# Performance work log

Measured on AMD Instinct MI355X. Metric: run time of the kernel, lower is better.

Reference implementation:

```python
import jax, jax.numpy as jnp
import numpy as np

B, T, C = 2, 2048, 2048
NH, HS = 16, 128          # heads, head_size = C // NH
NLQ, NLKV = 512, 512      # q / kv latent dims
DHR = 64                  # decoupled rope head dim


def _rope_cos_sin(T, dhr, dtype=jnp.float32):
    inv = 1.0 / (10000.0 ** (np.arange(0, dhr, 2, dtype=np.float32) / dhr))
    ang = np.arange(T, dtype=np.float32)[:, None] * inv[None, :]  # [T, dhr//2]
    return jnp.asarray(np.cos(ang), dtype), jnp.asarray(np.sin(ang), dtype)


def setup_inputs() -> dict:
    key = jax.random.key(0)
    ks = jax.random.split(key, 10)
    s = 0.02
    cos, sin = _rope_cos_sin(T, DHR)
    return {
        "x":     jax.random.normal(ks[0], (B, T, C), jnp.float32),
        "cos":   cos,
        "sin":   sin,
        "W_dq":  s * jax.random.normal(ks[1], (NLQ, C), jnp.float32),
        "W_uq":  s * jax.random.normal(ks[2], (C, NLQ), jnp.float32),
        "W_dkv": s * jax.random.normal(ks[3], (NLKV, C), jnp.float32),
        "W_uk":  s * jax.random.normal(ks[4], (C, NLKV), jnp.float32),
        "W_uv":  s * jax.random.normal(ks[5], (C, NLKV), jnp.float32),
        "W_qr":  s * jax.random.normal(ks[6], (NH * DHR, NLQ), jnp.float32),
        "W_kr":  s * jax.random.normal(ks[7], (DHR, C), jnp.float32),
        "W_o":   s * jax.random.normal(ks[8], (C, C), jnp.float32),
    }


def _apply_rope(x, cos, sin):
    # x: [B, T, H, D]; pairs are interleaved (even=real, odd=imag)
    xr = x.reshape(x.shape[:-1] + (-1, 2))
    re, im = xr[..., 0], xr[..., 1]
    c = cos[None, :, None, :]
    s = sin[None, :, None, :]
    out = jnp.stack([re * c - im * s, re * s + im * c], axis=-1)
    return out.reshape(x.shape)


def reference(x, cos, sin, W_dq, W_uq, W_dkv, W_uk, W_uv, W_qr, W_kr, W_o):
    b, t, c = x.shape
    nh, hs, nlq, nlkv, dhr = NH, HS, NLQ, NLKV, DHR
    scale = 1.0 / np.sqrt(hs + dhr).astype(np.float32)

    # low-rank latents
    c_q = x @ W_dq.T          # [B, T, nlq]
    c_kv = x @ W_dkv.T        # [B, T, nlkv]

    # absorbed matrices (training path)
    # W_uq: [C, nlq] viewed as [nlq, nh, hs]; W_uk: [C, nlkv] viewed as [nh, hs, nlkv]
    k_eff = jnp.einsum('qhd,hdk->hqk', W_uq.reshape(nlq, nh, hs),
                       W_uk.reshape(nh, hs, nlkv))              # [nh, nlq, nlkv]
    v_eff = (W_uv.T @ W_o.T).reshape(nlkv, nh, hs).transpose(1, 0, 2)  # [nh, nlkv, hs]

    # content scores via absorbed low-rank path
    qk = jnp.einsum('btq,hqk->bhtk', c_q, k_eff)                # [B, nh, T, nlkv]
    attn_c = jnp.einsum('bhtk,bsk->bhts', qk, c_kv)             # [B, nh, T, T]

    # decoupled RoPE scores
    c_kr = (x @ W_kr.T)[:, :, None, :]                          # [B, T, 1, dhr]
    k_r = _apply_rope(c_kr, cos, sin)[:, :, 0, :]               # [B, T, dhr]
    c_qr = (c_q @ W_qr.T).reshape(b, t, nh, dhr)
    q_r = _apply_rope(c_qr, cos, sin)                            # [B, T, nh, dhr]
    attn_r = jnp.einsum('bthd,bsd->bhts', q_r, k_r)             # [B, nh, T, T]

    attn = (attn_c + attn_r) * scale
    mask = jnp.tril(jnp.ones((t, t), dtype=bool))
    attn = jnp.where(mask[None, None], attn, -jnp.inf)
    p = jax.nn.softmax(attn, axis=-1)

    ctx = jnp.einsum('bhts,bsk->bhtk', p, c_kv)                 # [B, nh, T, nlkv]
    y = jnp.einsum('bhtk,hkd->bthd', ctx, v_eff).reshape(b, t, c)
    return y
```

## Files before the change

### kernel.cpp

```cpp
#include <hip/hip_runtime.h>
#include <hip/hip_bf16.h>
#include <math.h>

typedef long long ll;
typedef unsigned short ushort_t;
typedef __attribute__((ext_vector_type(8))) __bf16 bf16x8;
typedef __attribute__((ext_vector_type(4))) float f32x4;

__device__ __forceinline__ ushort_t f2bf(float f) {
    __hip_bfloat16 h = __float2bfloat16(f);
    return *reinterpret_cast<ushort_t*>(&h);
}
__device__ __forceinline__ float bf2f(ushort_t u) {
    return __uint_as_float(((unsigned)u) << 16);
}
__device__ __forceinline__ void stage16(const void* g_lane, void* lds_uniform) {
    __builtin_amdgcn_global_load_lds(
        (const __attribute__((address_space(1))) unsigned int*)g_lane,
        (__attribute__((address_space(3))) unsigned int*)lds_uniform, 16, 0, 0);
}

#define DPPMAX(v, ctrl) v = fmaxf(v, __uint_as_float((unsigned)__builtin_amdgcn_update_dpp( \
        0, (int)__float_as_uint(v), (ctrl), 0xF, 0xF, true)))
#define DPPADD(v, ctrl) v = v + __uint_as_float((unsigned)__builtin_amdgcn_update_dpp( \
        0, (int)__float_as_uint(v), (ctrl), 0xF, 0xF, true))
__device__ __forceinline__ float red_max16(float v) {
    DPPMAX(v, 0xB1); DPPMAX(v, 0x4E); DPPMAX(v, 0x141); DPPMAX(v, 0x140); return v;
}
__device__ __forceinline__ float red_sum16(float v) {
    DPPADD(v, 0xB1); DPPADD(v, 0x4E); DPPADD(v, 0x141); DPPADD(v, 0x140); return v;
}

#define TM 128
#define TN 128
#define TK 64

__global__ __launch_bounds__(256)
void gemm_bf16(const ushort_t* __restrict__ Ab, const ushort_t* __restrict__ Bb,
               void* __restrict__ Cb,
               int M, int N, int K,
               int a_rs, int b_rs, int c_rs, int Z2,
               ll a_bs1, ll a_bs2, ll b_bs1, ll b_bs2, ll c_bs1, ll c_bs2,
               int out_f32)
{
    const int m0 = blockIdx.y * TM;
    const int n0 = blockIdx.x * TN;
    const int z1 = blockIdx.z / Z2, z2 = blockIdx.z % Z2;

    const ushort_t* A = Ab + z1 * a_bs1 + z2 * a_bs2;
    const ushort_t* B = Bb + z1 * b_bs1 + z2 * b_bs2;

    __shared__ ushort_t As[2][TM][TK];
    __shared__ ushort_t Bs[2][TN][TK];

    const int tid  = threadIdx.x;
    const int w    = tid >> 6;
    const int l    = tid & 63;
    const int lo16 = l & 15;
    const int quad = l >> 4;
    const int wm0  = (w & 1) * 64;
    const int wn0  = (w >> 1) * 64;

    const int srow  = l >> 3;
    const int sunit = (l & 7) ^ srow;

    f32x4 acc[4][4];
    const f32x4 zero = {0.f, 0.f, 0.f, 0.f};
#pragma unroll
    for (int mi = 0; mi < 4; ++mi)
#pragma unroll
        for (int nj = 0; nj < 4; ++nj) acc[mi][nj] = zero;

    const int nIter = K / TK;

#pragma unroll
    for (int i = 0; i < 4; ++i) {
        const int rr = w * 32 + i * 8;
        stage16(A + (ll)(m0 + rr + srow) * a_rs + sunit * 8, &As[0][rr][0]);
        stage16(B + (ll)(n0 + rr + srow) * b_rs + sunit * 8, &Bs[0][rr][0]);
    }

    int buf = 0;
    for (int it = 0; it < nIter; ++it) {
        __syncthreads();
        if (it + 1 < nIter) {
            const int k0 = (it + 1) * TK;
            const int nb = buf ^ 1;
#pragma unroll
            for (int i = 0; i < 4; ++i) {
                const int rr = w * 32 + i * 8;
                stage16(A + (ll)(m0 + rr + srow) * a_rs + (k0 + sunit * 8), &As[nb][rr][0]);
                stage16(B + (ll)(n0 + rr + srow) * b_rs + (k0 + sunit * 8), &Bs[nb][rr][0]);
            }
        }
#pragma unroll
        for (int h = 0; h < 2; ++h) {
            const int phys = (h * 4 + quad) ^ (lo16 & 7);
            bf16x8 af[4], bfr[4];
#pragma unroll
            for (int mi = 0; mi < 4; ++mi)
                af[mi] = *(const bf16x8*)&As[buf][wm0 + mi * 16 + lo16][phys * 8];
#pragma unroll
            for (int nj = 0; nj < 4; ++nj)
                bfr[nj] = *(const bf16x8*)&Bs[buf][wn0 + nj * 16 + lo16][phys * 8];
#pragma unroll
            for (int mi = 0; mi < 4; ++mi)
#pragma unroll
                for (int nj = 0; nj < 4; ++nj)
                    acc[mi][nj] = __builtin_amdgcn_mfma_f32_16x16x32_bf16(
                        af[mi], bfr[nj], acc[mi][nj], 0, 0, 0);
        }
        buf ^= 1;
    }

    if (out_f32) {
        float* C = (float*)Cb + z1 * c_bs1 + z2 * c_bs2;
#pragma unroll
        for (int mi = 0; mi < 4; ++mi)
#pragma unroll
            for (int r = 0; r < 4; ++r) {
                const ll row = m0 + wm0 + mi * 16 + quad * 4 + r;
                float* cr = C + row * (ll)c_rs + (n0 + wn0 + lo16);
#pragma unroll
                for (int nj = 0; nj < 4; ++nj) cr[nj * 16] = acc[mi][nj][r];
            }
    } else {
        ushort_t* C = (ushort_t*)Cb + z1 * c_bs1 + z2 * c_bs2;
#pragma unroll
        for (int mi = 0; mi < 4; ++mi)
#pragma unroll
            for (int r = 0; r < 4; ++r) {
                const ll row = m0 + wm0 + mi * 16 + quad * 4 + r;
                ushort_t* cr = C + row * (ll)c_rs + (n0 + wn0 + lo16);
#pragma unroll
                for (int nj = 0; nj < 4; ++nj) cr[nj * 16] = f2bf(acc[mi][nj][r]);
            }
    }
}

#define QP_RS 3072
#define XP_RS 1152

__global__ __launch_bounds__(512)
void flash_mla(const ushort_t* __restrict__ QP,
               const ushort_t* __restrict__ WukT,
               const ushort_t* __restrict__ XP,
               const ushort_t* __restrict__ VT,
               float* __restrict__ out,
               float scale)
{
    const int h  = blockIdx.y;
    const int b  = blockIdx.z;

    __shared__ __align__(16) char smem[98304];
    ushort_t* Bw = (ushort_t*)smem;
    ushort_t* Q3 = (ushort_t*)(smem + 16384);

    const int tid  = threadIdx.x;
    const int w    = tid >> 6;
    const int g    = w >> 2;
    const int wl   = w & 3;
    const int l    = tid & 63;
    const int lo16 = l & 15;
    const int quad = l >> 4;
    char* Pw = smem + 90112 + w * 1024;

#pragma unroll 1
    for (int task = 0; task < 2; ++task) {
        const int jj = task ? (int)blockIdx.x : 15 - (int)blockIdx.x;
        const int qt = 2 * jj + g;
        const int t0 = qt * 64;
        const int nst = 4 * jj + 4;
        const int myLast = 2 * qt + (wl >> 1);

        __syncthreads();

        bf16x8 qa[18];

#pragma unroll
        for (int i = 0; i < 2; ++i) {
            int p = w * 128 + i * 64 + l;
            int r = p >> 4, u = p & 15, ul = u ^ (r & 15);
            stage16(WukT + ((ll)h * 512 + r) * 128 + ul * 8,
                    (char*)Bw + (ll)(w * 128 + i * 64) * 16);
        }
        bf16x8 ab[4];
#pragma unroll
        for (int kd = 0; kd < 4; ++kd)
            ab[kd] = *(const bf16x8*)(QP + (ll)(b * 2048 + t0 + 16 * wl + lo16) * QP_RS +
                                      h * 128 + kd * 32 + quad * 8);
        __syncthreads();

        for (int kc = 0; kc < 8; ++kc) {
#pragma unroll
            for (int nt = 0; nt < 4; ++nt) {
                f32x4 c = {0.f, 0.f, 0.f, 0.f};
#pragma unroll
                for (int kd = 0; kd < 4; ++kd) {
                    bf16x8 bb = *(const bf16x8*)(Bw + (nt * 16 + lo16) * 128 +
                                                 (((kd * 4 + quad) ^ lo16) & 15) * 8);
                    c = __builtin_amdgcn_mfma_f32_16x16x32_bf16(ab[kd], bb, c, 0, 0, 0);
                }
#pragma unroll
                for (int r = 0; r < 4; ++r)
                    Q3[(w * 16 + quad * 4 + r) * 72 + nt * 16 + lo16] = f2bf(c[r]);
            }
#pragma unroll
            for (int kd2 = 0; kd2 < 2; ++kd2)
                qa[kc * 2 + kd2] = *(const bf16x8*)(Q3 + (w * 16 + lo16) * 72 + kd2 * 32 + quad * 8);

            if (kc < 7) {
                __syncthreads();
#pragma unroll
                for (int i = 0; i < 2; ++i) {
                    int p = w * 128 + i * 64 + l;
                    int r = p >> 4, u = p & 15, ul = u ^ (r & 15);
                    stage16(WukT + ((ll)h * 512 + (kc + 1) * 64 + r) * 128 + ul * 8,
                            (char*)Bw + (ll)(w * 128 + i * 64) * 16);
                }
                __syncthreads();
            }
        }
#pragma unroll
        for (int kt = 16; kt < 18; ++kt)
            qa[kt] = *(const bf16x8*)(QP + (ll)(b * 2048 + t0 + 16 * wl + lo16) * QP_RS +
                                      2048 + h * 64 + (kt - 16) * 32 + quad * 8);

        f32x4 oacc[8];
        const f32x4 zero = {0.f, 0.f, 0.f, 0.f};
#pragma unroll
        for (int dt = 0; dt < 8; ++dt) oacc[dt] = zero;
        float mrow[4], lrow[4];
#pragma unroll
        for (int r = 0; r < 4; ++r) { mrow[r] = -3.0e38f; lrow[r] = 0.f; }

        __syncthreads();

        if (w < 6) {
#pragma unroll
            for (int i = 0; i < 6; ++i) {
                int p = w * 384 + i * 64 + l;
                int r = p / 72, u = p % 72, ul = u ^ (r & 7);
                stage16(XP + (ll)(b * 2048 + r) * XP_RS + 512 + ul * 8,
                        smem + (ll)(w * 384 + i * 64) * 16);
            }
        } else {
#pragma unroll
            for (int i = 0; i < 4; ++i) {
                int p = (w - 6) * 256 + i * 64 + l;
                int r = p >> 2, u = p & 3, ul = u ^ (r & 3);
                stage16(VT + ((ll)(b * 16 + h) * 128 + r) * 2048 + ul * 8,
                        smem + 73728 + (ll)((w - 6) * 256 + i * 64) * 16);
            }
        }

        int buf = 0;
        for (int st = 0; st < nst; ++st) {
            __syncthreads();

            if (st + 1 < nst) {
                const int s0n = (st + 1) * 32;
                const int nb = buf ^ 1;
                if (w < 6) {
                    char* ksn = smem + nb * 36864;
#pragma unroll
                    for (int i = 0; i < 6; ++i) {
                        int p = w * 384 + i * 64 + l;
                        int r = p / 72, u = p % 72, ul = u ^ (r & 7);
                        stage16(XP + (ll)(b * 2048 + s0n + r) * XP_RS + 512 + ul * 8,
                                ksn + (ll)(w * 384 + i * 64) * 16);
                    }
                } else {
                    char* vsn = smem + 73728 + nb * 8192;
#pragma unroll
                    for (int i = 0; i < 4; ++i) {
                        int p = (w - 6) * 256 + i * 64 + l;
                        int r = p >> 2, u = p & 3, ul = u ^ (r & 3);
                        stage16(VT + ((ll)(b * 16 + h) * 128 + r) * 2048 + s0n + ul * 8,
                                vsn + (ll)((w - 6) * 256 + i * 64) * 16);
                    }
                }
            }

            if (st <= myLast) {
                const int s0 = st * 32;
                const ushort_t* Ks = (const ushort_t*)(smem + buf * 36864);
                const ushort_t* Vs = (const ushort_t*)(smem + 73728 + buf * 8192);

                f32x4 sc[2];
                sc[0] = zero; sc[1] = zero;
                __builtin_amdgcn_s_setprio(1);
#pragma unroll
                for (int kt = 0; kt < 18; ++kt)
#pragma unroll
                    for (int nt = 0; nt < 2; ++nt) {
                        int phys = (kt * 4 + quad) ^ (lo16 & 7);
                        bf16x8 kb = *(const bf16x8*)(Ks + (nt * 16 + lo16) * 576 + phys * 8);
                        sc[nt] = __builtin_amdgcn_mfma_f32_16x16x32_bf16(qa[kt], kb, sc[nt], 0, 0, 0);
                    }
                __builtin_amdgcn_s_setprio(0);

                const int rbase = 16 * wl + quad * 4;
#pragma unroll
                for (int nt = 0; nt < 2; ++nt)
#pragma unroll
                    for (int r = 0; r < 4; ++r) sc[nt][r] *= scale;
                if (st >= 2 * qt) {
#pragma unroll
                    for (int nt = 0; nt < 2; ++nt)
#pragma unroll
                        for (int r = 0; r < 4; ++r)
                            if ((s0 + nt * 16 + lo16) > (t0 + rbase + r))
                                sc[nt][r] = -INFINITY;
                }

                float alpha[4];
#pragma unroll
                for (int r = 0; r < 4; ++r) {
                    float tm = red_max16(fmaxf(sc[0][r], sc[1][r]));
                    float mnew = fmaxf(mrow[r], tm);
                    alpha[r] = __expf(mrow[r] - mnew);
                    mrow[r] = mnew;
                    sc[0][r] = __expf(sc[0][r] - mnew);
                    sc[1][r] = __expf(sc[1][r] - mnew);
                    float rs = red_sum16(sc[0][r] + sc[1][r]);
                    lrow[r] = lrow[r] * alpha[r] + rs;
                }
#pragma unroll
                for (int dt = 0; dt < 8; ++dt)
#pragma unroll
                    for (int r = 0; r < 4; ++r) oacc[dt][r] *= alpha[r];

#pragma unroll
                for (int nt = 0; nt < 2; ++nt)
#pragma unroll
                    for (int r = 0; r < 4; ++r) {
                        int row = quad * 4 + r;
                        int col = nt * 16 + lo16;
                        *(ushort_t*)(Pw + row * 64 + (((col >> 3) ^ (row & 3)) << 4) + (col & 7) * 2)
                            = f2bf(sc[nt][r]);
                    }
                bf16x8 pf = *(const bf16x8*)(Pw + lo16 * 64 + (quad ^ (lo16 & 3)) * 16);

                __builtin_amdgcn_s_setprio(1);
#pragma unroll
                for (int dt = 0; dt < 8; ++dt) {
                    int phys = quad ^ (lo16 & 3);
                    bf16x8 vb = *(const bf16x8*)(Vs + (dt * 16 + lo16) * 32 + phys * 8);
                    oacc[dt] = __builtin_amdgcn_mfma_f32_16x16x32_bf16(pf, vb, oacc[dt], 0, 0, 0);
                }
                __builtin_amdgcn_s_setprio(0);
            }
            buf ^= 1;
        }

#pragma unroll
        for (int r = 0; r < 4; ++r) {
            const float inv = 1.0f / lrow[r];
            const ll row = (ll)(b * 2048 + t0 + 16 * wl + quad * 4 + r);
#pragma unroll
            for (int dt = 0; dt < 8; ++dt)
                out[row * 2048 + h * 128 + dt * 16 + lo16] = oacc[dt][r] * inv;
        }
    }
}

__global__ void cvt_f32_bf16(const float* __restrict__ in, ushort_t* __restrict__ out, ll n4)
{
    ll i = (ll)blockIdx.x * 256 + threadIdx.x;
    if (i >= n4) return;
    float4 v = *(const float4*)(in + i * 4);
    ushort4 u;
    u.x = f2bf(v.x); u.y = f2bf(v.y); u.z = f2bf(v.z); u.w = f2bf(v.w);
    *(ushort4*)(out + i * 4) = u;
}

__global__ void build_wb1(const float* __restrict__ Wdq, const float* __restrict__ Wdkv,
                          const float* __restrict__ Wkr, ushort_t* __restrict__ out)
{
    ll i4 = ((ll)blockIdx.x * 256 + threadIdx.x) * 4;
    if (i4 >= (ll)1152 * 2048) return;
    int row = (int)(i4 >> 11);
    int col = (int)(i4 & 2047);
    float4 v = make_float4(0.f, 0.f, 0.f, 0.f);
    if (row < 512)       v = *(const float4*)(Wdq + (ll)row * 2048 + col);
    else if (row < 1024) v = *(const float4*)(Wdkv + (ll)(row - 512) * 2048 + col);
    else if (row < 1088) v = *(const float4*)(Wkr + (ll)(row - 1024) * 2048 + col);
    ushort4 u;
    u.x = f2bf(v.x); u.y = f2bf(v.y); u.z = f2bf(v.z); u.w = f2bf(v.w);
    *(ushort4*)(out + i4) = u;
}

__global__ void transpose_f32_bf16(const float* __restrict__ in, ushort_t* __restrict__ out,
                                   int R, int C, ll in_bs, ll out_bs)
{
    __shared__ float tile[32][33];
    const float* I = in + (ll)blockIdx.z * in_bs;
    ushort_t*    O = out + (ll)blockIdx.z * out_bs;
    int r0 = blockIdx.y * 32, c0 = blockIdx.x * 32;
    int tx = threadIdx.x & 31, ty = threadIdx.x >> 5;
#pragma unroll
    for (int i = 0; i < 4; ++i)
        tile[ty + i * 8][tx] = I[(ll)(r0 + ty + i * 8) * C + (c0 + tx)];
    __syncthreads();
#pragma unroll
    for (int i = 0; i < 4; ++i)
        O[(ll)(c0 + ty + i * 8) * R + (r0 + tx)] = f2bf(tile[tx][ty + i * 8]);
}

__global__ void rope_kr(ushort_t* __restrict__ XP, const float* __restrict__ cb,
                        const float* __restrict__ sb)
{
    int idx = blockIdx.x * 256 + threadIdx.x;
    if (idx >= 2 * 2048 * 32) return;
    int j = idx & 31, t = (idx >> 5) & 2047, b = idx >> 16;
    float c = cb[t * 32 + j], s = sb[t * 32 + j];
    ushort_t* p = XP + ((ll)(b * 2048 + t)) * 1152 + 1024 + 2 * j;
    float re = bf2f(p[0]), im = bf2f(p[1]);
    p[0] = f2bf(re * c - im * s);
    p[1] = f2bf(re * s + im * c);
}

__global__ void rope_qr_ip(ushort_t* __restrict__ QP, const float* __restrict__ cb,
                           const float* __restrict__ sb)
{
    int idx = blockIdx.x * 256 + threadIdx.x;
    if (idx >= 4096 * 512) return;
    int pj = idx & 511, h = pj >> 5, j = pj & 31;
    int row = idx >> 9;
    int t = row & 2047;
    float c = cb[t * 32 + j], s = sb[t * 32 + j];
    ll base = (ll)row * 3072 + 2048 + h * 64 + 2 * j;
    float re = bf2f(QP[base]), im = bf2f(QP[base + 1]);
    QP[base]     = f2bf(re * c - im * s);
    QP[base + 1] = f2bf(re * s + im * c);
}

static inline void gemmb(hipStream_t st, const ushort_t* A, const ushort_t* B, void* C,
                         int M, int N, int K, int a_rs, int b_rs, int c_rs,
                         int nb, int Z2,
                         ll a_bs1, ll a_bs2, ll b_bs1, ll b_bs2, ll c_bs1, ll c_bs2,
                         int of32)
{
    dim3 g(N / TN, M / TM, nb);
    gemm_bf16<<<g, 256, 0, st>>>(A, B, C, M, N, K, a_rs, b_rs, c_rs, Z2,
                                 a_bs1, a_bs2, b_bs1, b_bs2, c_bs1, c_bs2, of32);
}

extern "C" void kernel_launch(void* const* d_in, const int* in_sizes, int n_in,
                              void* d_out, int out_size, void* d_ws, size_t ws_size,
                              hipStream_t stream)
{
    const float* x     = (const float*)d_in[0];
    const float* cosb  = (const float*)d_in[1];
    const float* sinb  = (const float*)d_in[2];
    const float* W_dq  = (const float*)d_in[3];
    const float* W_uq  = (const float*)d_in[4];
    const float* W_dkv = (const float*)d_in[5];
    const float* W_uk  = (const float*)d_in[6];
    const float* W_uv  = (const float*)d_in[7];
    const float* W_qr  = (const float*)d_in[8];
    const float* W_kr  = (const float*)d_in[9];
    const float* W_o   = (const float*)d_in[10];
    float* out = (float*)d_out;

    const float scale = 0.07216878364870323f;

    char* base = (char*)d_ws;
    ushort_t* WB1     = (ushort_t*)(base + 0);
    ushort_t* WukT_b  = (ushort_t*)(base + 4718592);
    ushort_t* WuvT_b  = (ushort_t*)(base + 6815744);
    ushort_t* WB2     = (ushort_t*)(base + 8912896);
    ushort_t* veffT_b = (ushort_t*)(base + 12058624);
    ushort_t* Wo_b    = (ushort_t*)(base + 14155776);
    ushort_t* xb      = (ushort_t*)(base + 22544384);
    ushort_t* XP      = (ushort_t*)(base + 39321600);
    ushort_t* VT_all  = (ushort_t*)(base + 48758784);
    ushort_t* QP      = (ushort_t*)(base + 65536000);

    cvt_f32_bf16<<<8192, 256, 0, stream>>>(x, xb, 2097152);
    cvt_f32_bf16<<<4096, 256, 0, stream>>>(W_o, Wo_b, 1048576);
    build_wb1<<<2304, 256, 0, stream>>>(W_dq, W_dkv, W_kr, WB1);
    transpose_f32_bf16<<<dim3(16, 4, 16), 256, 0, stream>>>(W_uk, WukT_b, 128, 512, 65536, 65536);
    transpose_f32_bf16<<<dim3(16, 64, 1), 256, 0, stream>>>(W_uv, WuvT_b, 2048, 512, 0, 0);
    transpose_f32_bf16<<<dim3(64, 16, 1), 256, 0, stream>>>(W_uq, WB2, 512, 2048, 0, 0);
    cvt_f32_bf16<<<512, 256, 0, stream>>>(W_qr, WB2 + (ll)2048 * 512, 131072);

    gemmb(stream, Wo_b, WuvT_b, veffT_b, 128, 512, 2048, 2048, 2048, 512,
          16, 16, 0, 262144, 0, 0, 0, 65536, 0);

    gemmb(stream, xb, WB1, XP, 4096, 1152, 2048, 2048, 2048, 1152,
          1, 1, 0, 0, 0, 0, 0, 0, 0);
    rope_kr<<<512, 256, 0, stream>>>(XP, cosb, sinb);

    gemmb(stream, veffT_b, XP + 512, VT_all, 128, 2048, 512, 512, 1152, 2048,
          32, 16, 0, 65536, (ll)2048 * 1152, 0, (ll)16 * 262144, 262144, 0);

    gemmb(stream, XP, WB2, QP, 4096, 3072, 512, 1152, 512, 3072,
          1, 1, 0, 0, 0, 0, 0, 0, 0);
    rope_qr_ip<<<8192, 256, 0, stream>>>(QP, cosb, sinb);

    flash_mla<<<dim3(8, 16, 2), 512, 0, stream>>>(QP, WukT_b, XP, VT_all, out, scale);

    (void)in_sizes; (void)n_in; (void)out_size; (void)ws_size;
}
```

Before: 440.2 us.

## Fuse prep kernels, split-K the v_eff GEMM, double-buffer W_uk staging in flash_mla

Merges the seven conversion and transpose kernels into one prep_all launch to cut launch overhead. The v_eff GEMM is split four ways along K into an fp32 scratch buffer, followed by a reduction kernel, to expose more parallelism for a small-M GEMM. In flash_mla the W_uk tile staging is double-buffered, so the next chunk loads while the current one is consumed, removing one barrier per iteration. The scratch reuses the VT_all region, and the LDS layout shifts to fit two W_uk buffers.

```diff
diff --git a/kernel.cpp b/kernel.cpp
--- a/kernel.cpp
+++ b/kernel.cpp
@@ -138,6 +138,102 @@
     }
 }
 
+__global__ __launch_bounds__(256)
+void prep_all(const float* __restrict__ x,    const float* __restrict__ Wo,
+              const float* __restrict__ Wdq,  const float* __restrict__ Wdkv,
+              const float* __restrict__ Wkr,  const float* __restrict__ Wuk,
+              const float* __restrict__ Wuv,  const float* __restrict__ Wuq,
+              const float* __restrict__ Wqr,
+              ushort_t* __restrict__ xb,   ushort_t* __restrict__ Wo_b,
+              ushort_t* __restrict__ WB1,  ushort_t* __restrict__ WukT,
+              ushort_t* __restrict__ WuvT, ushort_t* __restrict__ WB2)
+{
+    __shared__ float tile[32][33];
+    int bid = blockIdx.x;
+    const int tid = threadIdx.x;
+
+    if (bid < 8192) {
+        ll i = (ll)bid * 256 + tid;
+        float4 v = *(const float4*)(x + i * 4);
+        ushort4 u;
+        u.x = f2bf(v.x); u.y = f2bf(v.y); u.z = f2bf(v.z); u.w = f2bf(v.w);
+        *(ushort4*)(xb + i * 4) = u;
+        return;
+    }
+    bid -= 8192;
+    if (bid < 4096) {
+        ll i = (ll)bid * 256 + tid;
+        float4 v = *(const float4*)(Wo + i * 4);
+        ushort4 u;
+        u.x = f2bf(v.x); u.y = f2bf(v.y); u.z = f2bf(v.z); u.w = f2bf(v.w);
+        *(ushort4*)(Wo_b + i * 4) = u;
+        return;
+    }
+    bid -= 4096;
+    if (bid < 2304) {
+        ll i4 = ((ll)bid * 256 + tid) * 4;
+        int row = (int)(i4 >> 11);
+        int col = (int)(i4 & 2047);
+        float4 v = make_float4(0.f, 0.f, 0.f, 0.f);
+        if (row < 512)       v = *(const float4*)(Wdq + (ll)row * 2048 + col);
+        else if (row < 1024) v = *(const float4*)(Wdkv + (ll)(row - 512) * 2048 + col);
+        else if (row < 1088) v = *(const float4*)(Wkr + (ll)(row - 1024) * 2048 + col);
+        ushort4 u;
+        u.x = f2bf(v.x); u.y = f2bf(v.y); u.z = f2bf(v.z); u.w = f2bf(v.w);
+        *(ushort4*)(WB1 + i4) = u;
+        return;
+    }
+    bid -= 2304;
+    if (bid < 512) {
+        ll i = (ll)bid * 256 + tid;
+        float4 v = *(const float4*)(Wqr + i * 4);
+        ushort4 u;
+        u.x = f2bf(v.x); u.y = f2bf(v.y); u.z = f2bf(v.z); u.w = f2bf(v.w);
+        *(ushort4*)(WB2 + (ll)2048 * 512 + i * 4) = u;
+        return;
+    }
+    bid -= 512;
+
+    const float* I; ushort_t* O; int R, C, r0, c0;
+    if (bid < 1024) {
+        int bx = bid & 15, by = (bid >> 4) & 3, bz = bid >> 6;
+        I = Wuk + (ll)bz * 65536; O = WukT + (ll)bz * 65536;
+        R = 128; C = 512; r0 = by * 32; c0 = bx * 32;
+    } else if (bid < 2048) {
+        int b2 = bid - 1024;
+        I = Wuv; O = WuvT; R = 2048; C = 512;
+        r0 = (b2 >> 4) * 32; c0 = (b2 & 15) * 32;
+    } else {
+        int b2 = bid - 2048;
+        I = Wuq; O = WB2; R = 512; C = 2048;
+        r0 = (b2 >> 6) * 32; c0 = (b2 & 63) * 32;
+    }
+    int tx = tid & 31, ty = tid >> 5;
+#pragma unroll
+    for (int i = 0; i < 4; ++i)
+        tile[ty + i * 8][tx] = I[(ll)(r0 + ty + i * 8) * C + (c0 + tx)];
+    __syncthreads();
+#pragma unroll
+    for (int i = 0; i < 4; ++i)
+        O[(ll)(c0 + ty + i * 8) * R + (r0 + tx)] = f2bf(tile[tx][ty + i * 8]);
+}
+
+__global__ __launch_bounds__(256)
+void reduce_veff(const float* __restrict__ s, ushort_t* __restrict__ out)
+{
+    ll i = ((ll)blockIdx.x * 256 + threadIdx.x) * 4;
+    float4 a = *(const float4*)(s + i);
+    float4 b = *(const float4*)(s + 1048576 + i);
+    float4 c = *(const float4*)(s + 2097152 + i);
+    float4 d = *(const float4*)(s + 3145728 + i);
+    ushort4 u;
+    u.x = f2bf(a.x + b.x + c.x + d.x);
+    u.y = f2bf(a.y + b.y + c.y + d.y);
+    u.z = f2bf(a.z + b.z + c.z + d.z);
+    u.w = f2bf(a.w + b.w + c.w + d.w);
+    *(ushort4*)(out + i) = u;
+}
+
 #define QP_RS 3072
 #define XP_RS 1152
 
@@ -153,7 +249,6 @@
     const int b  = blockIdx.z;
 
     __shared__ __align__(16) char smem[98304];
-    ushort_t* Bw = (ushort_t*)smem;
     ushort_t* Q3 = (ushort_t*)(smem + 16384);
 
     const int tid  = threadIdx.x;
@@ -182,7 +277,7 @@
             int p = w * 128 + i * 64 + l;
             int r = p >> 4, u = p & 15, ul = u ^ (r & 15);
             stage16(WukT + ((ll)h * 512 + r) * 128 + ul * 8,
-                    (char*)Bw + (ll)(w * 128 + i * 64) * 16);
+                    smem + 36864 + (ll)(w * 128 + i * 64) * 16);
         }
         bf16x8 ab[4];
 #pragma unroll
@@ -191,35 +286,38 @@
                                       h * 128 + kd * 32 + quad * 8);
         __syncthreads();
 
+        int bwb = 0;
         for (int kc = 0; kc < 8; ++kc) {
-#pragma unroll
-            for (int nt = 0; nt < 4; ++nt) {
-                f32x4 c = {0.f, 0.f, 0.f, 0.f};
-#pragma unroll
-                for (int kd = 0; kd < 4; ++kd) {
-                    bf16x8 bb = *(const bf16x8*)(Bw + (nt * 16 + lo16) * 128 +
-                                                 (((kd * 4 + quad) ^ lo16) & 15) * 8);
-                    c = __builtin_amdgcn_mfma_f32_16x16x32_bf16(ab[kd], bb, c, 0, 0, 0);
-                }
-#pragma unroll
-                for (int r = 0; r < 4; ++r)
-                    Q3[(w * 16 + quad * 4 + r) * 72 + nt * 16 + lo16] = f2bf(c[r]);
-            }
-#pragma unroll
-            for (int kd2 = 0; kd2 < 2; ++kd2)
-                qa[kc * 2 + kd2] = *(const bf16x8*)(Q3 + (w * 16 + lo16) * 72 + kd2 * 32 + quad * 8);
-
             if (kc < 7) {
-                __syncthreads();
+                char* bwn = smem + 36864 + (ll)(bwb ^ 1) * 16384;
 #pragma unroll
                 for (int i = 0; i < 2; ++i) {
                     int p = w * 128 + i * 64 + l;
                     int r = p >> 4, u = p & 15, ul = u ^ (r & 15);
                     stage16(WukT + ((ll)h * 512 + (kc + 1) * 64 + r) * 128 + ul * 8,
-                            (char*)Bw + (ll)(w * 128 + i * 64) * 16);
+                            bwn + (ll)(w * 128 + i * 64) * 16);
                 }
-                __syncthreads();
-            }
+            }
+            const ushort_t* BwC = (const ushort_t*)(smem + 36864 + (ll)bwb * 16384);
+#pragma unroll
+            for (int nt = 0; nt < 4; ++nt) {
+                f32x4 c = {0.f, 0.f, 0.f, 0.f};
+#pragma unroll
+                for (int kd = 0; kd < 4; ++kd) {
+                    bf16x8 bb = *(const bf16x8*)(BwC + (nt * 16 + lo16) * 128 +
+                                                 (((kd * 4 + quad) ^ lo16) & 15) * 8);
+                    c = __builtin_amdgcn_mfma_f32_16x16x32_bf16(ab[kd], bb, c, 0, 0, 0);
+                }
+#pragma unroll
+                for (int r = 0; r < 4; ++r)
+                    Q3[(w * 16 + quad * 4 + r) * 72 + nt * 16 + lo16] = f2bf(c[r]);
+            }
+#pragma unroll
+            for (int kd2 = 0; kd2 < 2; ++kd2)
+                qa[kc * 2 + kd2] = *(const bf16x8*)(Q3 + (w * 16 + lo16) * 72 + kd2 * 32 + quad * 8);
+
+            __syncthreads();
+            bwb ^= 1;
         }
 #pragma unroll
         for (int kt = 16; kt < 18; ++kt)
@@ -233,8 +331,6 @@
         float mrow[4], lrow[4];
 #pragma unroll
         for (int r = 0; r < 4; ++r) { mrow[r] = -3.0e38f; lrow[r] = 0.f; }
-
-        __syncthreads();
 
         if (w < 6) {
 #pragma unroll
@@ -363,49 +459,6 @@
                 out[row * 2048 + h * 128 + dt * 16 + lo16] = oacc[dt][r] * inv;
         }
     }
-}
-
-__global__ void cvt_f32_bf16(const float* __restrict__ in, ushort_t* __restrict__ out, ll n4)
-{
-    ll i = (ll)blockIdx.x * 256 + threadIdx.x;
-    if (i >= n4) return;
-    float4 v = *(const float4*)(in + i * 4);
-    ushort4 u;
-    u.x = f2bf(v.x); u.y = f2bf(v.y); u.z = f2bf(v.z); u.w = f2bf(v.w);
-    *(ushort4*)(out + i * 4) = u;
-}
-
-__global__ void build_wb1(const float* __restrict__ Wdq, const float* __restrict__ Wdkv,
-                          const float* __restrict__ Wkr, ushort_t* __restrict__ out)
-{
-    ll i4 = ((ll)blockIdx.x * 256 + threadIdx.x) * 4;
-    if (i4 >= (ll)1152 * 2048) return;
-    int row = (int)(i4 >> 11);
-    int col = (int)(i4 & 2047);
-    float4 v = make_float4(0.f, 0.f, 0.f, 0.f);
-    if (row < 512)       v = *(const float4*)(Wdq + (ll)row * 2048 + col);
-    else if (row < 1024) v = *(const float4*)(Wdkv + (ll)(row - 512) * 2048 + col);
-    else if (row < 1088) v = *(const float4*)(Wkr + (ll)(row - 1024) * 2048 + col);
-    ushort4 u;
-    u.x = f2bf(v.x); u.y = f2bf(v.y); u.z = f2bf(v.z); u.w = f2bf(v.w);
-    *(ushort4*)(out + i4) = u;
-}
-
-__global__ void transpose_f32_bf16(const float* __restrict__ in, ushort_t* __restrict__ out,
-                                   int R, int C, ll in_bs, ll out_bs)
-{
-    __shared__ float tile[32][33];
-    const float* I = in + (ll)blockIdx.z * in_bs;
-    ushort_t*    O = out + (ll)blockIdx.z * out_bs;
-    int r0 = blockIdx.y * 32, c0 = blockIdx.x * 32;
-    int tx = threadIdx.x & 31, ty = threadIdx.x >> 5;
-#pragma unroll
-    for (int i = 0; i < 4; ++i)
-        tile[ty + i * 8][tx] = I[(ll)(r0 + ty + i * 8) * C + (c0 + tx)];
-    __syncthreads();
-#pragma unroll
-    for (int i = 0; i < 4; ++i)
-        O[(ll)(c0 + ty + i * 8) * R + (r0 + tx)] = f2bf(tile[tx][ty + i * 8]);
 }
 
 __global__ void rope_kr(ushort_t* __restrict__ XP, const float* __restrict__ cb,
@@ -477,17 +530,14 @@
     ushort_t* XP      = (ushort_t*)(base + 39321600);
     ushort_t* VT_all  = (ushort_t*)(base + 48758784);
     ushort_t* QP      = (ushort_t*)(base + 65536000);
-
-    cvt_f32_bf16<<<8192, 256, 0, stream>>>(x, xb, 2097152);
-    cvt_f32_bf16<<<4096, 256, 0, stream>>>(W_o, Wo_b, 1048576);
-    build_wb1<<<2304, 256, 0, stream>>>(W_dq, W_dkv, W_kr, WB1);
-    transpose_f32_bf16<<<dim3(16, 4, 16), 256, 0, stream>>>(W_uk, WukT_b, 128, 512, 65536, 65536);
-    transpose_f32_bf16<<<dim3(16, 64, 1), 256, 0, stream>>>(W_uv, WuvT_b, 2048, 512, 0, 0);
-    transpose_f32_bf16<<<dim3(64, 16, 1), 256, 0, stream>>>(W_uq, WB2, 512, 2048, 0, 0);
-    cvt_f32_bf16<<<512, 256, 0, stream>>>(W_qr, WB2 + (ll)2048 * 512, 131072);
-
-    gemmb(stream, Wo_b, WuvT_b, veffT_b, 128, 512, 2048, 2048, 2048, 512,
-          16, 16, 0, 262144, 0, 0, 0, 65536, 0);
+    float*    VTscr   = (float*)(base + 48758784);
+
+    prep_all<<<18176, 256, 0, stream>>>(x, W_o, W_dq, W_dkv, W_kr, W_uk, W_uv, W_uq,
+                                        W_qr, xb, Wo_b, WB1, WukT_b, WuvT_b, WB2);
+
+    gemmb(stream, Wo_b, WuvT_b, VTscr, 128, 512, 512, 2048, 2048, 512,
+          64, 16, 512, 262144, 512, 0, 1048576, 65536, 1);
+    reduce_veff<<<1024, 256, 0, stream>>>(VTscr, veffT_b);
 
     gemmb(stream, xb, WB1, XP, 4096, 1152, 2048, 2048, 2048, 1152,
           1, 1, 0, 0, 0, 0, 0, 0, 0);
```

New measurement: 412.6 us. 1.07x faster.
